# Optimization experiments

Measured on AMD Instinct MI355X. Metric: run time of the kernel, lower is better.

Reference implementation:

```python
import jax, jax.numpy as jnp
from jax import lax
import numpy as np

N_HOS, N_TYPES, N_STRUCTS = 4, 16, 512
N_COMBOS = N_HOS * N_TYPES  # 64
HID = 1024
N_ITERS = 60  # fixed PDHG iterations (differentiable unrolled solver)


def setup_inputs() -> dict:
    key = jax.random.key(0)
    ks = jax.random.split(key, 8)
    X = jax.random.uniform(ks[0], (2048, N_HOS, N_TYPES), dtype=jnp.float32)
    # sparse 0/1 structure matrix; guarantee each structure touches >=1 combo
    S = (jax.random.uniform(ks[1], (N_COMBOS, N_STRUCTS)) < 0.08).astype(jnp.float32)
    cols = jnp.arange(N_STRUCTS)
    S = S.at[cols % N_COMBOS, cols].set(1.0)
    # MLP params (He-ish init)
    W1 = jax.random.normal(ks[2], (N_COMBOS, HID), dtype=jnp.float32) * (2.0 / N_COMBOS) ** 0.5
    b1 = jnp.zeros((HID,), jnp.float32)
    W2 = jax.random.normal(ks[3], (HID, HID), dtype=jnp.float32) * (2.0 / HID) ** 0.5
    b2 = jnp.zeros((HID,), jnp.float32)
    W3 = jax.random.normal(ks[4], (HID, N_STRUCTS), dtype=jnp.float32) * (2.0 / HID) ** 0.5
    b3 = jnp.zeros((N_STRUCTS,), jnp.float32)
    return {"X": X, "W1": W1, "b1": b1, "W2": W2, "b2": b2,
            "W3": W3, "b3": b3, "S": S, "batch_size": 2048}


def nn_forward(X, W1, b1, W2, b2, W3, b3):
    # torch loop applies act_fun after EVERY layer, including the last
    Z = X.reshape(X.shape[0], -1)                 # [B, n_hos*n_types]
    Z = jax.nn.relu(Z @ W1 + b1)
    Z = jax.nn.relu(Z @ W2 + b2)
    Z = jax.nn.relu(Z @ W3 + b3)                  # [B, n_structures]
    return Z


def solve_lp(S, W, B, Z, n_iters=N_ITERS):
    """Batched solve of: max_x W.x - ||x - Z||_2  s.t. x >= 0, S x <= B.
    PDHG (Chambolle-Pock) on  min_x f(x) + i{Kx <= c},
    f(x) = -W.x + ||x - Z||_2,  K = [S; -I],  c = [B; 0].
    Same optimization problem as the CvxpyLayer, solved by a fixed-iteration
    batched primal-dual method (differentiable via unrolling)."""
    batch, n = Z.shape
    m = S.shape[0]

    # ||K||_2 via power iteration on K^T K = S^T S + I (constant wrt params)
    def pow_step(v, _):
        v2 = S.T @ (S @ v) + v
        return v2 / jnp.linalg.norm(v2), None
    v0 = jnp.full((n,), 1.0 / np.sqrt(n), Z.dtype)
    v, _ = lax.scan(pow_step, v0, None, length=30)
    L = jnp.sqrt(jnp.vdot(v, S.T @ (S @ v) + v))
    L = lax.stop_gradient(L)
    tau = 0.9 / L
    sigma = 0.9 / L

    c = jnp.concatenate([B, jnp.zeros_like(Z)], axis=-1)  # [B, m+n]

    def Kx(x):
        return jnp.concatenate([x @ S.T, -x], axis=-1)    # [B, m+n]

    def KTy(y):
        return y[:, :m] @ S - y[:, m:]                    # [B, n]

    def prox_f(v):
        # argmin_x 1/(2 tau) ||x - v||^2 - W.x + ||x - Z||_2
        u = v + tau * W
        d = u - Z
        nrm = jnp.linalg.norm(d, axis=-1, keepdims=True)
        scale = jnp.maximum(1.0 - tau / jnp.maximum(nrm, 1e-12), 0.0)
        return Z + scale * d

    def step(carry, _):
        x, xbar, y = carry
        y = jnp.maximum(y + sigma * (Kx(xbar) - c), 0.0)
        x_new = prox_f(x - tau * KTy(y))
        xbar = 2.0 * x_new - x
        return (x_new, xbar, y), None

    x0 = jnp.zeros_like(Z)
    y0 = jnp.zeros((batch, m + n), Z.dtype)
    (x, _, _), _ = lax.scan(step, (x0, x0, y0), None, length=n_iters)
    return x


def reference(X, W1, b1, W2, b2, W3, b3, S, batch_size):
    Z = nn_forward(X, W1, b1, W2, b2, W3, b3)     # [B, n_structures]
    W = jnp.ones_like(Z)                          # weights w = 1 (as in torch)
    B = X.reshape(batch_size, -1)                 # capacities b
    return solve_lp(S, W, B, Z)
```

## Files before the change

### kernel.cpp

```cpp
#include <hip/hip_runtime.h>


typedef _Float16 half8 __attribute__((ext_vector_type(8)));
typedef __fp16 fp16x2 __attribute__((ext_vector_type(2)));
typedef __fp16 fp16x4 __attribute__((ext_vector_type(4)));
typedef float floatx4 __attribute__((ext_vector_type(4)));
typedef float floatx2 __attribute__((ext_vector_type(2)));

#define BATCH 2048
#define NITERS 60
#define XBS 520
#define YLS 72

typedef const __attribute__((address_space(1))) unsigned int* gptr_as1;
typedef __attribute__((address_space(3))) unsigned int* lptr_as3;
__device__ __forceinline__ void gl_lds16(const _Float16* g, _Float16* s) {
    __builtin_amdgcn_global_load_lds((gptr_as1)g, (lptr_as3)s, 16, 0, 0);
}

template <int CTRL>
__device__ __forceinline__ float dpp_addf(float x) {
    int y = __builtin_amdgcn_update_dpp(0, __builtin_bit_cast(int, x), CTRL, 0xf, 0xf, true);
    return x + __builtin_bit_cast(float, y);
}
__device__ __forceinline__ float sum16(float x) {
    x = dpp_addf<0xB1>(x);
    x = dpp_addf<0x4E>(x);
    x = dpp_addf<0x124>(x);
    x = dpp_addf<0x128>(x);
    return x;
}
__device__ __forceinline__ float sum64(float x) {
    x = sum16(x);
    x += __builtin_bit_cast(float, __builtin_amdgcn_ds_swizzle(__builtin_bit_cast(int, x), 0x401F));
    x += __shfl_xor(x, 32, 64);
    return x;
}

__device__ void power_64(const float* __restrict__ S, float* __restrict__ tau_g) {
    __shared__ unsigned long long rowm[64][8];
    __shared__ float G[64][65];
    __shared__ float wl[64], pg[4][64];
    int t = threadIdx.x, wv = t >> 6, ln = t & 63;
    for (int rr = 0; rr < 16; rr++) {
        int r = wv * 16 + rr;
        float v[8];
#pragma unroll
        for (int e = 0; e < 8; e++) v[e] = S[r * 512 + e * 64 + ln];
#pragma unroll
        for (int e = 0; e < 8; e++) {
            unsigned long long m = __ballot(v[e] != 0.f);
            if (ln == 0) rowm[r][e] = m;
        }
    }
    __syncthreads();
    for (int k = 0; k < 16; k++) {
        int idx = t * 16 + k;
        int i = idx >> 6, j = idx & 63;
        int cnt = 0;
#pragma unroll
        for (int e = 0; e < 8; e++) cnt += __popcll(rowm[i][e] & rowm[j][e]);
        G[i][j] = (float)cnt;
    }
    if (wv == 0) {
        int cnt = 0;
#pragma unroll
        for (int e = 0; e < 8; e++) cnt += __popcll(rowm[ln][e]);
        wl[ln] = (float)cnt * 0.044194173824159216f;
    }
    __syncthreads();
    for (int s = 0; s < 30; s++) {
        float a = 0.f;
#pragma unroll
        for (int jj = 0; jj < 16; jj++) {
            int j = wv * 16 + jj;
            a += G[ln][j] * wl[j];
        }
        pg[wv][ln] = a;
        __syncthreads();
        if (wv == 0) {
            float g = (pg[0][ln] + pg[1][ln]) + (pg[2][ln] + pg[3][ln]);
            float wi = wl[ln];
            float s1 = sum64(wi * g);
            float s2 = sum64(wi * wi);
            float n = sqrtf(s1 + 2.f * s2 + 1.f);
            wl[ln] = (g + wi) / n;
        }
        __syncthreads();
    }
    if (wv == 0) {
        float wi = wl[ln];
        float s2 = sum64(wi * wi);
        if (ln == 0) tau_g[0] = 0.9f / sqrtf(s2 + 1.f);
    }
}

__global__ __launch_bounds__(256) void prep(
    const float* __restrict__ X, _Float16* __restrict__ Xh,
    const float* __restrict__ W1, _Float16* __restrict__ W1t,
    const float* __restrict__ W2, _Float16* __restrict__ W2t,
    const float* __restrict__ W3, _Float16* __restrict__ W3t,
    const float* __restrict__ S, _Float16* __restrict__ s1f,
    _Float16* __restrict__ s2f) {
    __shared__ float tile[32][33];
    int tid = threadIdx.x;
    int bid = blockIdx.x;
    if (bid < 512) {
        int i = bid * 256 + tid;
        Xh[i] = (_Float16)X[i];
        return;
    }
    bid -= 512;
    if (bid < 1600) {
        const float* W; _Float16* Wt; int K, N, b;
        if (bid < 64)        { W = W1; Wt = W1t; K = 64;   N = 1024; b = bid; }
        else if (bid < 1088) { W = W2; Wt = W2t; K = 1024; N = 1024; b = bid - 64; }
        else                 { W = W3; Wt = W3t; K = 1024; N = 512;  b = bid - 1088; }
        int nbx = N / 32;
        int n0 = (b % nbx) * 32, k0 = (b / nbx) * 32;
        int tx = tid & 31, ty = tid >> 5;
#pragma unroll
        for (int i = 0; i < 4; i++)
            tile[ty + i * 8][tx] = W[(size_t)(k0 + ty + i * 8) * N + n0 + tx];
        __syncthreads();
#pragma unroll
        for (int i = 0; i < 4; i++)
            Wt[(size_t)(n0 + ty + i * 8) * K + k0 + tx] = (_Float16)tile[tx][ty + i * 8];
        return;
    }
    bid -= 1600;
    int i = bid * 256 + tid;
    if (i < 4 * 16 * 64 * 8) {
        int j = i & 7, lane = (i >> 3) & 63, kk = (i >> 9) & 15, wc = i >> 13;
        int pos = kk * 32 + (lane >> 4) * 8 + j;
        int pp = pos >> 7, r = pos & 127;
        int hh = r >> 6, r2 = r & 63;
        int lmc = r2 >> 2, t3 = r2 & 3;
        int c = pp * 128 + (hh * 4 + t3) * 16 + lmc;
        int m = wc * 16 + (lane & 15);
        s1f[i] = (_Float16)S[m * 512 + c];
    } else {
        int i2 = i - 4 * 16 * 64 * 8;
        int j = i2 & 7, lane = (i2 >> 3) & 63, c = (i2 >> 9) & 1,
            tt = (i2 >> 10) & 7, wc = i2 >> 13;
        int kc = c * 32 + (lane >> 4) * 8 + j;
        int n = wc * 128 + tt * 16 + (lane & 15);
        s2f[i2] = (_Float16)S[kc * 512 + n];
    }
}

__global__ __launch_bounds__(256, 2) void gemm_relu(
    const _Float16* __restrict__ A, const _Float16* __restrict__ Wt,
    const float* __restrict__ bias, _Float16* __restrict__ outh,
    float* __restrict__ outf, int N, int K,
    const float* __restrict__ Sp, float* __restrict__ tau_g) {
    __shared__ __align__(16) _Float16 As[64 * 32];
    __shared__ __align__(16) _Float16 Bs[64 * 32];
    int tid = threadIdx.x;
    int bm = blockIdx.y * 64;
    int bn = blockIdx.x * 64;
    if (bn >= N) {
        if (blockIdx.y == 0 && Sp) power_64(Sp, tau_g);
        return;
    }
    int w = tid >> 6, l = tid & 63;
    int wr = w >> 1, wc = w & 1;
    int lm = l & 15, q = l >> 4;
    floatx4 acc[2][2] = {};

    int lc = l ^ ((l >> 3) & 7);
    int srow = w * 16 + (lc >> 2), scol = (lc & 3) * 8;
    const _Float16* ag = A + (size_t)(bm + srow) * K + scol;
    const _Float16* bg = Wt + (size_t)(bn + srow) * K + scol;
    _Float16* as = &As[(w * 16) * 32];
    _Float16* bs = &Bs[(w * 16) * 32];
    int sx = ((lm >> 1) & 7) << 3;

    for (int k0 = 0; k0 < K; k0 += 32) {
        gl_lds16(ag + k0, as);
        gl_lds16(bg + k0, bs);
        __syncthreads();
        half8 af[2], bf[2];
#pragma unroll
        for (int mt = 0; mt < 2; mt++)
            af[mt] = *(const half8*)&As[((wr * 32 + mt * 16 + lm) * 32 + q * 8) ^ sx];
#pragma unroll
        for (int nt = 0; nt < 2; nt++)
            bf[nt] = *(const half8*)&Bs[((wc * 32 + nt * 16 + lm) * 32 + q * 8) ^ sx];
#pragma unroll
        for (int mt = 0; mt < 2; mt++)
#pragma unroll
            for (int nt = 0; nt < 2; nt++)
                acc[mt][nt] = __builtin_amdgcn_mfma_f32_16x16x32_f16(
                    af[mt], bf[nt], acc[mt][nt], 0, 0, 0);
        __syncthreads();
    }
#pragma unroll
    for (int nt = 0; nt < 2; nt++) {
        int col = bn + wc * 32 + nt * 16 + lm;
        float bv = bias[col];
#pragma unroll
        for (int mt = 0; mt < 2; mt++) {
#pragma unroll
            for (int v = 0; v < 4; v++) {
                int row = bm + wr * 32 + mt * 16 + q * 4 + v;
                float val = fmaxf(acc[mt][nt][v] + bv, 0.f);
                if (outh) outh[(size_t)row * N + col] = (_Float16)val;
                else      outf[(size_t)row * N + col] = val;
            }
        }
    }
}

__global__ __launch_bounds__(256, 1) void pdhg_mfma(
    const float* __restrict__ Zb, const float* __restrict__ Xf,
    const _Float16* __restrict__ s1f, const _Float16* __restrict__ s2f,
    const float* __restrict__ tau_p, float* __restrict__ out) {
    __shared__ __align__(16) _Float16 xb_d[8 * XBS];
    __shared__ __align__(16) _Float16 yl_d[8 * YLS];
    __shared__ __align__(16) float red[8][4];
    int tid = threadIdx.x;
    int p = tid >> 6;
    int l = tid & 63, lm = l & 15, q = l >> 4;
    int lq = lm & 7;
    int qa = q & 1;
    int h = q >> 1;
    int b0 = blockIdx.x * 8;

    half8 s1[16], s2[8][2];
#pragma unroll
    for (int k = 0; k < 16; k++)
        s1[k] = *(const half8*)&s1f[((p * 16 + k) * 64 + l) * 8];
#pragma unroll
    for (int u = 0; u < 8; u++)
#pragma unroll
        for (int c = 0; c < 2; c++)
            s2[u][c] = *(const half8*)&s2f[(((p * 8 + u) * 2 + c) * 64 + l) * 8];

    floatx4 z4[4], tz4[4], x4[4], xb4[4], yh4[4], d4[4];
    floatx4 ylo = {}, Bc;
    floatx4 a1p[4] = {};
    floatx4 acc2[8] = {};
    const floatx4 zero4 = {0.f, 0.f, 0.f, 0.f};
    float tau = tau_p[0];
    float sig = tau;

#pragma unroll
    for (int v = 0; v < 4; v++)
        Bc[v] = Xf[(b0 + qa * 4 + v) * 64 + p * 16 + lm];
#pragma unroll
    for (int t = 0; t < 4; t++) {
#pragma unroll
        for (int v = 0; v < 4; v++) {
            float zz = Zb[(size_t)(b0 + qa * 4 + v) * 512 + p * 128 + (h * 4 + t) * 16 + lm];
            z4[t][v] = zz;
            tz4[t][v] = tau - zz;
        }
        x4[t] = zero4; xb4[t] = zero4; yh4[t] = zero4;
    }
    {
        half8 hz = {0, 0, 0, 0, 0, 0, 0, 0};
        for (int i = tid; i < (8 * XBS) / 8; i += 256)
            *(half8*)&xb_d[i * 8] = hz;
        for (int i = tid; i < 8 * YLS; i += 256)
            yl_d[i] = (_Float16)0.f;
    }
    __syncthreads();

#pragma unroll 1
    for (int it = 0; it < NITERS; ++it) {
#pragma unroll
        for (int k = 0; k < 16; k++) {
            half8 ad = *(const half8*)&xb_d[lq * XBS + k * 32 + q * 8];
            a1p[k & 3] = __builtin_amdgcn_mfma_f32_16x16x32_f16(ad, s1[k], a1p[k & 3], 0, 0, 0);
        }
        floatx4 a1 = (a1p[0] + a1p[1]) + (a1p[2] + a1p[3]);
        floatx4 yv = __builtin_elementwise_max(ylo + sig * (a1 - Bc), zero4);
        floatx4 dy = yv - ylo;
        ylo = yv;
        if (q < 2) {
#pragma unroll
            for (int v = 0; v < 4; v++)
                yl_d[(q * 4 + v) * YLS + p * 16 + lm] = (_Float16)dy[v];
        }
        __syncthreads();
        half8 a2d[2];
#pragma unroll
        for (int c = 0; c < 2; c++)
            a2d[c] = *(const half8*)&yl_d[lq * YLS + c * 32 + q * 8];
#pragma unroll
        for (int u = 0; u < 8; u++)
#pragma unroll
            for (int c = 0; c < 2; c++)
                acc2[u] = __builtin_amdgcn_mfma_f32_16x16x32_f16(a2d[c], s2[u][c], acc2[u], 0, 0, 0);
        floatx4 pn = {};
#pragma unroll
        for (int t = 0; t < 4; t++) {
            floatx4 accs = h ? acc2[t + 4] : acc2[t];
            yh4[t] = __builtin_elementwise_max(yh4[t] - sig * xb4[t], zero4);
            floatx4 kty = accs - yh4[t];
            floatx4 dd = (x4[t] - tau * kty) + tz4[t];
            d4[t] = dd;
            pn += dd * dd;
        }
#pragma unroll
        for (int v = 0; v < 4; v++) pn[v] = sum16(pn[v]);
#pragma unroll
        for (int v = 0; v < 4; v++) pn[v] += __shfl_xor(pn[v], 32, 64);
        if (lm == 0 && q < 2) {
#pragma unroll
            for (int v = 0; v < 4; v++) red[q * 4 + v][p] = pn[v];
        }
        __syncthreads();
        floatx4 sv;
#pragma unroll
        for (int v = 0; v < 4; v++) {
            floatx4 rr = *(const floatx4*)&red[qa * 4 + v][0];
            float n2 = (rr.x + rr.y) + (rr.z + rr.w);
            sv[v] = fmaxf(1.f - tau * rsqrtf(fmaxf(n2, 1e-24f)), 0.f);
        }
#pragma unroll
        for (int t = 0; t < 4; t++) {
            floatx4 xn = z4[t] + sv * d4[t];
            floatx4 xbn = 2.f * xn - x4[t];
            d4[t] = xbn - xb4[t];
            x4[t] = xn;
            xb4[t] = xbn;
        }
#pragma unroll
        for (int v = 0; v < 4; v++) {
            fp16x2 p0 = __builtin_amdgcn_cvt_pkrtz(d4[0][v], d4[1][v]);
            fp16x2 p1 = __builtin_amdgcn_cvt_pkrtz(d4[2][v], d4[3][v]);
            fp16x4 hd = __builtin_shufflevector(p0, p1, 0, 1, 2, 3);
            *(fp16x4*)&xb_d[(qa * 4 + v) * XBS + p * 128 + h * 64 + lm * 4] = hd;
        }
        __syncthreads();
    }
#pragma unroll
    for (int t = 0; t < 4; t++)
#pragma unroll
        for (int v = 0; v < 4; v++)
            out[(size_t)(b0 + qa * 4 + v) * 512 + p * 128 + (h * 4 + t) * 16 + lm] = x4[t][v];
}

extern "C" void kernel_launch(void* const* d_in, const int* in_sizes, int n_in,
                              void* d_out, int out_size, void* d_ws, size_t ws_size,
                              hipStream_t stream) {
    const float* X  = (const float*)d_in[0];
    const float* W1 = (const float*)d_in[1];
    const float* b1 = (const float*)d_in[2];
    const float* W2 = (const float*)d_in[3];
    const float* b2 = (const float*)d_in[4];
    const float* W3 = (const float*)d_in[5];
    const float* b3 = (const float*)d_in[6];
    const float* S  = (const float*)d_in[7];
    float* out = (float*)d_out;

    char* ws = (char*)d_ws;
    size_t off = 0;
    auto alloc = [&](size_t bytes) {
        void* p = ws + off;
        off += (bytes + 255) & ~(size_t)255;
        return p;
    };
    _Float16* Xh  = (_Float16*)alloc((size_t)BATCH * 64 * 2);
    _Float16* W1t = (_Float16*)alloc((size_t)64 * 1024 * 2);
    _Float16* W2t = (_Float16*)alloc((size_t)1024 * 1024 * 2);
    _Float16* W3t = (_Float16*)alloc((size_t)1024 * 512 * 2);
    _Float16* H1  = (_Float16*)alloc((size_t)BATCH * 1024 * 2);
    _Float16* H2  = (_Float16*)alloc((size_t)BATCH * 1024 * 2);
    float*    Zb  = (float*)alloc((size_t)BATCH * 512 * 4);
    _Float16* s1f = (_Float16*)alloc((size_t)4 * 16 * 64 * 8 * 2);
    _Float16* s2f = (_Float16*)alloc((size_t)4 * 8 * 2 * 64 * 8 * 2);
    float*    tau = (float*)alloc(256);

    hipLaunchKernelGGL(prep, dim3(2368), dim3(256), 0, stream,
                       X, Xh, W1, W1t, W2, W2t, W3, W3t, S, s1f, s2f);
    hipLaunchKernelGGL(gemm_relu, dim3(16, 32), dim3(256), 0, stream,
                       Xh, W1t, b1, H1, (float*)nullptr, 1024, 64,
                       (const float*)nullptr, (float*)nullptr);
    hipLaunchKernelGGL(gemm_relu, dim3(17, 32), dim3(256), 0, stream,
                       H1, W2t, b2, H2, (float*)nullptr, 1024, 1024, S, tau);
    hipLaunchKernelGGL(gemm_relu, dim3(8, 32), dim3(256), 0, stream,
                       H2, W3t, b3, (_Float16*)nullptr, Zb, 512, 1024,
                       (const float*)nullptr, (float*)nullptr);
    hipLaunchKernelGGL(pdhg_mfma, dim3(BATCH / 8), dim3(256), 0, stream,
                       Zb, X, s1f, s2f, tau, out);
}
```

Measured before the change: 204.2 us.

## Fuse first MLP layer and power iteration into prep kernel, double-buffer GEMM

Computes the first MLP layer directly from fp32 X and W1 inside the prep kernel, converting to fp16 on the fly into LDS. This removes the separate X and W1 conversion passes and one kernel launch. The power iteration that computes tau moves into the same prep kernel instead of occupying an extra column of blocks in the layer-2 GEMM. The remaining GEMMs gain double-buffered LDS so the next K slab loads while MFMAs run on the current one. The cost is one fewer barrier-free overlap point and more LDS per block, which may lower occupancy.

```diff
diff --git a/kernel.cpp b/kernel.cpp
--- a/kernel.cpp
+++ b/kernel.cpp
@@ -37,10 +37,13 @@
     return x;
 }
 
-__device__ void power_64(const float* __restrict__ S, float* __restrict__ tau_g) {
-    __shared__ unsigned long long rowm[64][8];
-    __shared__ float G[64][65];
-    __shared__ float wl[64], pg[4][64];
+__device__ void power_64(const float* __restrict__ S, float* __restrict__ tau_g,
+                         char* smem) {
+    typedef unsigned long long ull;
+    ull (*rowm)[8] = (ull(*)[8])smem;
+    float (*G)[65] = (float(*)[65])(smem + 4096);
+    float* wl = (float*)(smem + 4096 + 16640);
+    float (*pg)[64] = (float(*)[64])(smem + 4096 + 16640 + 256);
     int t = threadIdx.x, wv = t >> 6, ln = t & 63;
     for (int rr = 0; rr < 16; rr++) {
         int r = wv * 16 + rr;
@@ -95,27 +98,81 @@
     }
 }
 
-__global__ __launch_bounds__(256) void prep(
-    const float* __restrict__ X, _Float16* __restrict__ Xh,
-    const float* __restrict__ W1, _Float16* __restrict__ W1t,
+__global__ __launch_bounds__(256) void head(
+    const float* __restrict__ X, const float* __restrict__ W1,
+    const float* __restrict__ b1, _Float16* __restrict__ H1,
     const float* __restrict__ W2, _Float16* __restrict__ W2t,
     const float* __restrict__ W3, _Float16* __restrict__ W3t,
     const float* __restrict__ S, _Float16* __restrict__ s1f,
-    _Float16* __restrict__ s2f) {
-    __shared__ float tile[32][33];
+    _Float16* __restrict__ s2f, float* __restrict__ tau_g) {
+    __shared__ __align__(16) char smem[22272];
     int tid = threadIdx.x;
     int bid = blockIdx.x;
     if (bid < 512) {
-        int i = bid * 256 + tid;
-        Xh[i] = (_Float16)X[i];
+        _Float16* As = (_Float16*)smem;
+        _Float16* Bs = (_Float16*)(smem + 8192);
+        int bm = (bid >> 4) * 64, bn = (bid & 15) * 64;
+        {
+            int r = tid >> 2, c0 = (tid & 3) * 16;
+            const float* xp = X + (size_t)(bm + r) * 64 + c0;
+            int sw = (r & 7) << 3;
+#pragma unroll
+            for (int i = 0; i < 4; i++) {
+                floatx4 v = *(const floatx4*)(xp + i * 4);
+                fp16x4 hh = {(__fp16)v.x, (__fp16)v.y, (__fp16)v.z, (__fp16)v.w};
+                *(fp16x4*)&As[r * 64 + ((c0 + i * 4) ^ sw)] = hh;
+            }
+            int nx = tid & 63, ky = (tid >> 6) * 16;
+            int swb = (nx & 7) << 3;
+#pragma unroll
+            for (int i = 0; i < 16; i++) {
+                float wv = W1[(size_t)(ky + i) * 1024 + bn + nx];
+                Bs[nx * 64 + ((ky + i) ^ swb)] = (_Float16)wv;
+            }
+        }
+        __syncthreads();
+        int w = tid >> 6, l = tid & 63;
+        int wr = w >> 1, wc = w & 1;
+        int lm = l & 15, q = l >> 4;
+        int sxa = (lm & 7) << 3;
+        floatx4 acc[2][2] = {};
+#pragma unroll
+        for (int k0 = 0; k0 < 64; k0 += 32) {
+            half8 af[2], bf[2];
+#pragma unroll
+            for (int mt = 0; mt < 2; mt++)
+                af[mt] = *(const half8*)&As[(wr * 32 + mt * 16 + lm) * 64 + ((k0 + q * 8) ^ sxa)];
+#pragma unroll
+            for (int nt = 0; nt < 2; nt++)
+                bf[nt] = *(const half8*)&Bs[(wc * 32 + nt * 16 + lm) * 64 + ((k0 + q * 8) ^ sxa)];
+#pragma unroll
+            for (int mt = 0; mt < 2; mt++)
+#pragma unroll
+                for (int nt = 0; nt < 2; nt++)
+                    acc[mt][nt] = __builtin_amdgcn_mfma_f32_16x16x32_f16(
+                        af[mt], bf[nt], acc[mt][nt], 0, 0, 0);
+        }
+#pragma unroll
+        for (int nt = 0; nt < 2; nt++) {
+            int col = bn + wc * 32 + nt * 16 + lm;
+            float bv = b1[col];
+#pragma unroll
+            for (int mt = 0; mt < 2; mt++)
+#pragma unroll
+                for (int v = 0; v < 4; v++) {
+                    int row = bm + wr * 32 + mt * 16 + q * 4 + v;
+                    H1[(size_t)row * 1024 + col] =
+                        (_Float16)fmaxf(acc[mt][nt][v] + bv, 0.f);
+                }
+        }
         return;
     }
     bid -= 512;
-    if (bid < 1600) {
+    if (bid < 1536) {
+        float (*tile)[33] = (float(*)[33])smem;
         const float* W; _Float16* Wt; int K, N, b;
-        if (bid < 64)        { W = W1; Wt = W1t; K = 64;   N = 1024; b = bid; }
-        else if (bid < 1088) { W = W2; Wt = W2t; K = 1024; N = 1024; b = bid - 64; }
-        else                 { W = W3; Wt = W3t; K = 1024; N = 512;  b = bid - 1088; }
+        if (bid < 1024) { W = W2; Wt = W2t; K = 1024; N = 1024; b = bid; }
+        else            { W = W3; Wt = W3t; K = 1024; N = 512;  b = bid - 1024; }
         int nbx = N / 32;
         int n0 = (b % nbx) * 32, k0 = (b / nbx) * 32;
         int tx = tid & 31, ty = tid >> 5;
@@ -128,41 +185,40 @@
             Wt[(size_t)(n0 + ty + i * 8) * K + k0 + tx] = (_Float16)tile[tx][ty + i * 8];
         return;
     }
-    bid -= 1600;
-    int i = bid * 256 + tid;
-    if (i < 4 * 16 * 64 * 8) {
-        int j = i & 7, lane = (i >> 3) & 63, kk = (i >> 9) & 15, wc = i >> 13;
-        int pos = kk * 32 + (lane >> 4) * 8 + j;
-        int pp = pos >> 7, r = pos & 127;
-        int hh = r >> 6, r2 = r & 63;
-        int lmc = r2 >> 2, t3 = r2 & 3;
-        int c = pp * 128 + (hh * 4 + t3) * 16 + lmc;
-        int m = wc * 16 + (lane & 15);
-        s1f[i] = (_Float16)S[m * 512 + c];
-    } else {
-        int i2 = i - 4 * 16 * 64 * 8;
-        int j = i2 & 7, lane = (i2 >> 3) & 63, c = (i2 >> 9) & 1,
-            tt = (i2 >> 10) & 7, wc = i2 >> 13;
-        int kc = c * 32 + (lane >> 4) * 8 + j;
-        int n = wc * 128 + tt * 16 + (lane & 15);
-        s2f[i2] = (_Float16)S[kc * 512 + n];
-    }
-}
-
-__global__ __launch_bounds__(256, 2) void gemm_relu(
+    bid -= 1536;
+    if (bid < 256) {
+        int i = bid * 256 + tid;
+        if (i < 4 * 16 * 64 * 8) {
+            int j = i & 7, lane = (i >> 3) & 63, kk = (i >> 9) & 15, wc = i >> 13;
+            int pos = kk * 32 + (lane >> 4) * 8 + j;
+            int pp = pos >> 7, r = pos & 127;
+            int hh = r >> 6, r2 = r & 63;
+            int lmc = r2 >> 2, t3 = r2 & 3;
+            int c = pp * 128 + (hh * 4 + t3) * 16 + lmc;
+            int m = wc * 16 + (lane & 15);
+            s1f[i] = (_Float16)S[m * 512 + c];
+        } else {
+            int i2 = i - 4 * 16 * 64 * 8;
+            int j = i2 & 7, lane = (i2 >> 3) & 63, c = (i2 >> 9) & 1,
+                tt = (i2 >> 10) & 7, wc = i2 >> 13;
+            int kc = c * 32 + (lane >> 4) * 8 + j;
+            int n = wc * 128 + tt * 16 + (lane & 15);
+            s2f[i2] = (_Float16)S[kc * 512 + n];
+        }
+        return;
+    }
+    power_64(S, tau_g, smem);
+}
+
+__global__ __launch_bounds__(256, 2) void gemm_relu_db(
     const _Float16* __restrict__ A, const _Float16* __restrict__ Wt,
     const float* __restrict__ bias, _Float16* __restrict__ outh,
-    float* __restrict__ outf, int N, int K,
-    const float* __restrict__ Sp, float* __restrict__ tau_g) {
-    __shared__ __align__(16) _Float16 As[64 * 32];
-    __shared__ __align__(16) _Float16 Bs[64 * 32];
+    float* __restrict__ outf, int N, int K) {
+    __shared__ __align__(16) _Float16 As[2][64 * 32];
+    __shared__ __align__(16) _Float16 Bs[2][64 * 32];
     int tid = threadIdx.x;
     int bm = blockIdx.y * 64;
     int bn = blockIdx.x * 64;
-    if (bn >= N) {
-        if (blockIdx.y == 0 && Sp) power_64(Sp, tau_g);
-        return;
-    }
     int w = tid >> 6, l = tid & 63;
     int wr = w >> 1, wc = w & 1;
     int lm = l & 15, q = l >> 4;
@@ -172,27 +228,53 @@
     int srow = w * 16 + (lc >> 2), scol = (lc & 3) * 8;
     const _Float16* ag = A + (size_t)(bm + srow) * K + scol;
     const _Float16* bg = Wt + (size_t)(bn + srow) * K + scol;
-    _Float16* as = &As[(w * 16) * 32];
-    _Float16* bs = &Bs[(w * 16) * 32];
+    _Float16* as0 = &As[0][(w * 16) * 32];
+    _Float16* bs0 = &Bs[0][(w * 16) * 32];
+    _Float16* as1 = &As[1][(w * 16) * 32];
+    _Float16* bs1 = &Bs[1][(w * 16) * 32];
     int sx = ((lm >> 1) & 7) << 3;
 
-    for (int k0 = 0; k0 < K; k0 += 32) {
-        gl_lds16(ag + k0, as);
-        gl_lds16(bg + k0, bs);
-        __syncthreads();
-        half8 af[2], bf[2];
-#pragma unroll
-        for (int mt = 0; mt < 2; mt++)
-            af[mt] = *(const half8*)&As[((wr * 32 + mt * 16 + lm) * 32 + q * 8) ^ sx];
-#pragma unroll
-        for (int nt = 0; nt < 2; nt++)
-            bf[nt] = *(const half8*)&Bs[((wc * 32 + nt * 16 + lm) * 32 + q * 8) ^ sx];
-#pragma unroll
-        for (int mt = 0; mt < 2; mt++)
+    gl_lds16(ag, as0);
+    gl_lds16(bg, bs0);
+    __syncthreads();
+    for (int k0 = 0; k0 < K; k0 += 64) {
+        gl_lds16(ag + k0 + 32, as1);
+        gl_lds16(bg + k0 + 32, bs1);
+        {
+            half8 af[2], bf[2];
+#pragma unroll
+            for (int mt = 0; mt < 2; mt++)
+                af[mt] = *(const half8*)&As[0][((wr * 32 + mt * 16 + lm) * 32 + q * 8) ^ sx];
 #pragma unroll
             for (int nt = 0; nt < 2; nt++)
-                acc[mt][nt] = __builtin_amdgcn_mfma_f32_16x16x32_f16(
-                    af[mt], bf[nt], acc[mt][nt], 0, 0, 0);
+                bf[nt] = *(const half8*)&Bs[0][((wc * 32 + nt * 16 + lm) * 32 + q * 8) ^ sx];
+#pragma unroll
+            for (int mt = 0; mt < 2; mt++)
+#pragma unroll
+                for (int nt = 0; nt < 2; nt++)
+                    acc[mt][nt] = __builtin_amdgcn_mfma_f32_16x16x32_f16(
+                        af[mt], bf[nt], acc[mt][nt], 0, 0, 0);
+        }
+        __syncthreads();
+        if (k0 + 64 < K) {
+            gl_lds16(ag + k0 + 64, as0);
+            gl_lds16(bg + k0 + 64, bs0);
+        }
+        {
+            half8 af[2], bf[2];
+#pragma unroll
+            for (int mt = 0; mt < 2; mt++)
+                af[mt] = *(const half8*)&As[1][((wr * 32 + mt * 16 + lm) * 32 + q * 8) ^ sx];
+#pragma unroll
+            for (int nt = 0; nt < 2; nt++)
+                bf[nt] = *(const half8*)&Bs[1][((wc * 32 + nt * 16 + lm) * 32 + q * 8) ^ sx];
+#pragma unroll
+            for (int mt = 0; mt < 2; mt++)
+#pragma unroll
+                for (int nt = 0; nt < 2; nt++)
+                    acc[mt][nt] = __builtin_amdgcn_mfma_f32_16x16x32_f16(
+                        af[mt], bf[nt], acc[mt][nt], 0, 0, 0);
+        }
         __syncthreads();
     }
 #pragma unroll
@@ -363,8 +445,6 @@
         off += (bytes + 255) & ~(size_t)255;
         return p;
     };
-    _Float16* Xh  = (_Float16*)alloc((size_t)BATCH * 64 * 2);
-    _Float16* W1t = (_Float16*)alloc((size_t)64 * 1024 * 2);
     _Float16* W2t = (_Float16*)alloc((size_t)1024 * 1024 * 2);
     _Float16* W3t = (_Float16*)alloc((size_t)1024 * 512 * 2);
     _Float16* H1  = (_Float16*)alloc((size_t)BATCH * 1024 * 2);
@@ -374,16 +454,12 @@
     _Float16* s2f = (_Float16*)alloc((size_t)4 * 8 * 2 * 64 * 8 * 2);
     float*    tau = (float*)alloc(256);
 
-    hipLaunchKernelGGL(prep, dim3(2368), dim3(256), 0, stream,
-                       X, Xh, W1, W1t, W2, W2t, W3, W3t, S, s1f, s2f);
-    hipLaunchKernelGGL(gemm_relu, dim3(16, 32), dim3(256), 0, stream,
-                       Xh, W1t, b1, H1, (float*)nullptr, 1024, 64,
-                       (const float*)nullptr, (float*)nullptr);
-    hipLaunchKernelGGL(gemm_relu, dim3(17, 32), dim3(256), 0, stream,
-                       H1, W2t, b2, H2, (float*)nullptr, 1024, 1024, S, tau);
-    hipLaunchKernelGGL(gemm_relu, dim3(8, 32), dim3(256), 0, stream,
-                       H2, W3t, b3, (_Float16*)nullptr, Zb, 512, 1024,
-                       (const float*)nullptr, (float*)nullptr);
+    hipLaunchKernelGGL(head, dim3(2305), dim3(256), 0, stream,
+                       X, W1, b1, H1, W2, W2t, W3, W3t, S, s1f, s2f, tau);
+    hipLaunchKernelGGL(gemm_relu_db, dim3(16, 32), dim3(256), 0, stream,
+                       H1, W2t, b2, H2, (float*)nullptr, 1024, 1024);
+    hipLaunchKernelGGL(gemm_relu_db, dim3(8, 32), dim3(256), 0, stream,
+                       H2, W3t, b3, (_Float16*)nullptr, Zb, 512, 1024);
     hipLaunchKernelGGL(pdhg_mfma, dim3(BATCH / 8), dim3(256), 0, stream,
                        Zb, X, s1f, s2f, tau, out);
 }
```

Result: slower. 213.3 us (+4.5%).

## Fuse MLP layers into the PDHG kernel per 8-row batch tile

Applied to the files above, without the earlier changes.

Removes the three separate GEMM launches and the fp16 X conversion. Each 8-row PDHG block now computes its own MLP forward pass: H1 and H2 live in shared memory, and the final layer's output stays in registers as Z. This removes global round-trips for H1, H2 and Z and cuts kernel launches. The cost is that every block streams the full W2t and W3t matrices straight from global memory without LDS staging, and half of each 16-row MFMA tile is unused. The power iteration moves into the prep kernel as an extra block.

```diff
diff --git a/kernel.cpp b/kernel.cpp
--- a/kernel.cpp
+++ b/kernel.cpp
@@ -5,18 +5,12 @@
 typedef __fp16 fp16x2 __attribute__((ext_vector_type(2)));
 typedef __fp16 fp16x4 __attribute__((ext_vector_type(4)));
 typedef float floatx4 __attribute__((ext_vector_type(4)));
-typedef float floatx2 __attribute__((ext_vector_type(2)));
 
 #define BATCH 2048
 #define NITERS 60
 #define XBS 520
 #define YLS 72
-
-typedef const __attribute__((address_space(1))) unsigned int* gptr_as1;
-typedef __attribute__((address_space(3))) unsigned int* lptr_as3;
-__device__ __forceinline__ void gl_lds16(const _Float16* g, _Float16* s) {
-    __builtin_amdgcn_global_load_lds((gptr_as1)g, (lptr_as3)s, 16, 0, 0);
-}
+#define H1S 1032
 
 template <int CTRL>
 __device__ __forceinline__ float dpp_addf(float x) {
@@ -96,21 +90,14 @@
 }
 
 __global__ __launch_bounds__(256) void prep(
-    const float* __restrict__ X, _Float16* __restrict__ Xh,
     const float* __restrict__ W1, _Float16* __restrict__ W1t,
     const float* __restrict__ W2, _Float16* __restrict__ W2t,
     const float* __restrict__ W3, _Float16* __restrict__ W3t,
     const float* __restrict__ S, _Float16* __restrict__ s1f,
-    _Float16* __restrict__ s2f) {
+    _Float16* __restrict__ s2f, float* __restrict__ tau_g) {
     __shared__ float tile[32][33];
     int tid = threadIdx.x;
     int bid = blockIdx.x;
-    if (bid < 512) {
-        int i = bid * 256 + tid;
-        Xh[i] = (_Float16)X[i];
-        return;
-    }
-    bid -= 512;
     if (bid < 1600) {
         const float* W; _Float16* Wt; int K, N, b;
         if (bid < 64)        { W = W1; Wt = W1t; K = 64;   N = 1024; b = bid; }
@@ -128,114 +115,149 @@
             Wt[(size_t)(n0 + ty + i * 8) * K + k0 + tx] = (_Float16)tile[tx][ty + i * 8];
         return;
     }
-    bid -= 1600;
-    int i = bid * 256 + tid;
-    if (i < 4 * 16 * 64 * 8) {
-        int j = i & 7, lane = (i >> 3) & 63, kk = (i >> 9) & 15, wc = i >> 13;
-        int pos = kk * 32 + (lane >> 4) * 8 + j;
-        int pp = pos >> 7, r = pos & 127;
-        int hh = r >> 6, r2 = r & 63;
-        int lmc = r2 >> 2, t3 = r2 & 3;
-        int c = pp * 128 + (hh * 4 + t3) * 16 + lmc;
-        int m = wc * 16 + (lane & 15);
-        s1f[i] = (_Float16)S[m * 512 + c];
-    } else {
-        int i2 = i - 4 * 16 * 64 * 8;
-        int j = i2 & 7, lane = (i2 >> 3) & 63, c = (i2 >> 9) & 1,
-            tt = (i2 >> 10) & 7, wc = i2 >> 13;
-        int kc = c * 32 + (lane >> 4) * 8 + j;
-        int n = wc * 128 + tt * 16 + (lane & 15);
-        s2f[i2] = (_Float16)S[kc * 512 + n];
-    }
-}
-
-__global__ __launch_bounds__(256, 2) void gemm_relu(
-    const _Float16* __restrict__ A, const _Float16* __restrict__ Wt,
-    const float* __restrict__ bias, _Float16* __restrict__ outh,
-    float* __restrict__ outf, int N, int K,
-    const float* __restrict__ Sp, float* __restrict__ tau_g) {
-    __shared__ __align__(16) _Float16 As[64 * 32];
-    __shared__ __align__(16) _Float16 Bs[64 * 32];
-    int tid = threadIdx.x;
-    int bm = blockIdx.y * 64;
-    int bn = blockIdx.x * 64;
-    if (bn >= N) {
-        if (blockIdx.y == 0 && Sp) power_64(Sp, tau_g);
+    if (bid < 1856) {
+        int i = (bid - 1600) * 256 + tid;
+        if (i < 4 * 16 * 64 * 8) {
+            int j = i & 7, lane = (i >> 3) & 63, kk = (i >> 9) & 15, wc = i >> 13;
+            int pos = kk * 32 + (lane >> 4) * 8 + j;
+            int pp = pos >> 7, r = pos & 127;
+            int hh = r >> 6, r2 = r & 63;
+            int lmc = r2 >> 2, t3 = r2 & 3;
+            int c = pp * 128 + (hh * 4 + t3) * 16 + lmc;
+            int m = wc * 16 + (lane & 15);
+            s1f[i] = (_Float16)S[m * 512 + c];
+        } else {
+            int i2 = i - 4 * 16 * 64 * 8;
+            int j = i2 & 7, lane = (i2 >> 3) & 63, c = (i2 >> 9) & 1,
+                tt = (i2 >> 10) & 7, wc = i2 >> 13;
+            int kc = c * 32 + (lane >> 4) * 8 + j;
+            int n = wc * 128 + tt * 16 + (lane & 15);
+            s2f[i2] = (_Float16)S[kc * 512 + n];
+        }
         return;
     }
-    int w = tid >> 6, l = tid & 63;
-    int wr = w >> 1, wc = w & 1;
-    int lm = l & 15, q = l >> 4;
-    floatx4 acc[2][2] = {};
-
-    int lc = l ^ ((l >> 3) & 7);
-    int srow = w * 16 + (lc >> 2), scol = (lc & 3) * 8;
-    const _Float16* ag = A + (size_t)(bm + srow) * K + scol;
-    const _Float16* bg = Wt + (size_t)(bn + srow) * K + scol;
-    _Float16* as = &As[(w * 16) * 32];
-    _Float16* bs = &Bs[(w * 16) * 32];
-    int sx = ((lm >> 1) & 7) << 3;
-
-    for (int k0 = 0; k0 < K; k0 += 32) {
-        gl_lds16(ag + k0, as);
-        gl_lds16(bg + k0, bs);
-        __syncthreads();
-        half8 af[2], bf[2];
-#pragma unroll
-        for (int mt = 0; mt < 2; mt++)
-            af[mt] = *(const half8*)&As[((wr * 32 + mt * 16 + lm) * 32 + q * 8) ^ sx];
-#pragma unroll
-        for (int nt = 0; nt < 2; nt++)
-            bf[nt] = *(const half8*)&Bs[((wc * 32 + nt * 16 + lm) * 32 + q * 8) ^ sx];
-#pragma unroll
-        for (int mt = 0; mt < 2; mt++)
-#pragma unroll
-            for (int nt = 0; nt < 2; nt++)
-                acc[mt][nt] = __builtin_amdgcn_mfma_f32_16x16x32_f16(
-                    af[mt], bf[nt], acc[mt][nt], 0, 0, 0);
-        __syncthreads();
-    }
-#pragma unroll
-    for (int nt = 0; nt < 2; nt++) {
-        int col = bn + wc * 32 + nt * 16 + lm;
-        float bv = bias[col];
-#pragma unroll
-        for (int mt = 0; mt < 2; mt++) {
-#pragma unroll
-            for (int v = 0; v < 4; v++) {
-                int row = bm + wr * 32 + mt * 16 + q * 4 + v;
-                float val = fmaxf(acc[mt][nt][v] + bv, 0.f);
-                if (outh) outh[(size_t)row * N + col] = (_Float16)val;
-                else      outf[(size_t)row * N + col] = val;
-            }
-        }
-    }
-}
-
-__global__ __launch_bounds__(256, 1) void pdhg_mfma(
-    const float* __restrict__ Zb, const float* __restrict__ Xf,
+    power_64(S, tau_g);
+}
+
+__global__ __launch_bounds__(256, 1) void mega(
+    const float* __restrict__ X,
+    const _Float16* __restrict__ W1t, const float* __restrict__ b1,
+    const _Float16* __restrict__ W2t, const float* __restrict__ b2,
+    const _Float16* __restrict__ W3t, const float* __restrict__ b3,
     const _Float16* __restrict__ s1f, const _Float16* __restrict__ s2f,
     const float* __restrict__ tau_p, float* __restrict__ out) {
-    __shared__ __align__(16) _Float16 xb_d[8 * XBS];
-    __shared__ __align__(16) _Float16 yl_d[8 * YLS];
-    __shared__ __align__(16) float red[8][4];
+    __shared__ __align__(16) char smem[34304];
+    _Float16* H1 = (_Float16*)smem;
+    _Float16* H2 = (_Float16*)(smem + 16512);
+    _Float16* X8 = (_Float16*)(smem + 33024);
+    _Float16* xb_d = (_Float16*)smem;
+    _Float16* yl_d = (_Float16*)(smem + 8320);
+    float (*red)[4] = (float(*)[4])(smem + 9472);
+
     int tid = threadIdx.x;
-    int p = tid >> 6;
+    int wp = tid >> 6;
     int l = tid & 63, lm = l & 15, q = l >> 4;
     int lq = lm & 7;
-    int qa = q & 1;
-    int h = q >> 1;
+    int qa = q & 1, h = q >> 1;
     int b0 = blockIdx.x * 8;
 
+    if (tid < 128) {
+        int r = tid >> 4, c = (tid & 15) * 4;
+        floatx4 v = *(const floatx4*)&X[(size_t)(b0 + r) * 64 + c];
+        fp16x4 hh = {(__fp16)v.x, (__fp16)v.y, (__fp16)v.z, (__fp16)v.w};
+        *(fp16x4*)&X8[r * 72 + c] = hh;
+    }
+    __syncthreads();
+
+    {
+        floatx4 acc1[16] = {};
+#pragma unroll
+        for (int kk = 0; kk < 2; kk++) {
+            half8 a = *(const half8*)&X8[lq * 72 + kk * 32 + q * 8];
+#pragma unroll
+            for (int u = 0; u < 16; u++) {
+                int col = wp * 256 + u * 16 + lm;
+                half8 b = *(const half8*)&W1t[(size_t)col * 64 + kk * 32 + q * 8];
+                acc1[u] = __builtin_amdgcn_mfma_f32_16x16x32_f16(a, b, acc1[u], 0, 0, 0);
+            }
+        }
+        if (q < 2) {
+#pragma unroll
+            for (int u = 0; u < 16; u++) {
+                int col = wp * 256 + u * 16 + lm;
+                float bv = b1[col];
+#pragma unroll
+                for (int v = 0; v < 4; v++)
+                    H1[(q * 4 + v) * H1S + col] = (_Float16)fmaxf(acc1[u][v] + bv, 0.f);
+            }
+        }
+    }
+    __syncthreads();
+
+    {
+        floatx4 acc2h[16] = {};
+        half8 B2[16];
+#pragma unroll
+        for (int u = 0; u < 16; u++)
+            B2[u] = *(const half8*)&W2t[(size_t)(wp * 256 + u * 16 + lm) * 1024 + q * 8];
+        half8 a_cur = *(const half8*)&H1[lq * H1S + q * 8];
+#pragma unroll 1
+        for (int k0 = 0; k0 < 1024; k0 += 32) {
+            int knx = (k0 + 32) & 1023;
+            half8 a_nxt = *(const half8*)&H1[lq * H1S + knx + q * 8];
+#pragma unroll
+            for (int u = 0; u < 16; u++) {
+                half8 bn = *(const half8*)&W2t[(size_t)(wp * 256 + u * 16 + lm) * 1024 + knx + q * 8];
+                acc2h[u] = __builtin_amdgcn_mfma_f32_16x16x32_f16(a_cur, B2[u], acc2h[u], 0, 0, 0);
+                B2[u] = bn;
+            }
+            a_cur = a_nxt;
+        }
+        __syncthreads();
+        if (q < 2) {
+#pragma unroll
+            for (int u = 0; u < 16; u++) {
+                int col = wp * 256 + u * 16 + lm;
+                float bv = b2[col];
+#pragma unroll
+                for (int v = 0; v < 4; v++)
+                    H2[(q * 4 + v) * H1S + col] = (_Float16)fmaxf(acc2h[u][v] + bv, 0.f);
+            }
+        }
+    }
+    __syncthreads();
+
+    floatx4 acc3[8] = {};
+    {
+        half8 B3[8];
+#pragma unroll
+        for (int u = 0; u < 8; u++)
+            B3[u] = *(const half8*)&W3t[(size_t)(wp * 128 + u * 16 + lm) * 1024 + q * 8];
+        half8 a_cur = *(const half8*)&H2[lq * H1S + q * 8];
+#pragma unroll 1
+        for (int k0 = 0; k0 < 1024; k0 += 32) {
+            int knx = (k0 + 32) & 1023;
+            half8 a_nxt = *(const half8*)&H2[lq * H1S + knx + q * 8];
+#pragma unroll
+            for (int u = 0; u < 8; u++) {
+                half8 bn = *(const half8*)&W3t[(size_t)(wp * 128 + u * 16 + lm) * 1024 + knx + q * 8];
+                acc3[u] = __builtin_amdgcn_mfma_f32_16x16x32_f16(a_cur, B3[u], acc3[u], 0, 0, 0);
+                B3[u] = bn;
+            }
+            a_cur = a_nxt;
+        }
+    }
+    __syncthreads();
+
     half8 s1[16], s2[8][2];
 #pragma unroll
     for (int k = 0; k < 16; k++)
-        s1[k] = *(const half8*)&s1f[((p * 16 + k) * 64 + l) * 8];
+        s1[k] = *(const half8*)&s1f[((wp * 16 + k) * 64 + l) * 8];
 #pragma unroll
     for (int u = 0; u < 8; u++)
 #pragma unroll
         for (int c = 0; c < 2; c++)
-            s2[u][c] = *(const half8*)&s2f[(((p * 8 + u) * 2 + c) * 64 + l) * 8];
+            s2[u][c] = *(const half8*)&s2f[(((wp * 8 + u) * 2 + c) * 64 + l) * 8];
 
     floatx4 z4[4], tz4[4], x4[4], xb4[4], yh4[4], d4[4];
     floatx4 ylo = {}, Bc;
@@ -247,12 +269,14 @@
 
 #pragma unroll
     for (int v = 0; v < 4; v++)
-        Bc[v] = Xf[(b0 + qa * 4 + v) * 64 + p * 16 + lm];
+        Bc[v] = X[(size_t)(b0 + qa * 4 + v) * 64 + wp * 16 + lm];
 #pragma unroll
     for (int t = 0; t < 4; t++) {
+        int col = wp * 128 + (h * 4 + t) * 16 + lm;
+        float bv = b3[col];
 #pragma unroll
         for (int v = 0; v < 4; v++) {
-            float zz = Zb[(size_t)(b0 + qa * 4 + v) * 512 + p * 128 + (h * 4 + t) * 16 + lm];
+            float zz = fmaxf(acc3[h * 4 + t][v] + bv, 0.f);
             z4[t][v] = zz;
             tz4[t][v] = tau - zz;
         }
@@ -281,7 +305,7 @@
         if (q < 2) {
 #pragma unroll
             for (int v = 0; v < 4; v++)
-                yl_d[(q * 4 + v) * YLS + p * 16 + lm] = (_Float16)dy[v];
+                yl_d[(q * 4 + v) * YLS + wp * 16 + lm] = (_Float16)dy[v];
         }
         __syncthreads();
         half8 a2d[2];
@@ -309,7 +333,7 @@
         for (int v = 0; v < 4; v++) pn[v] += __shfl_xor(pn[v], 32, 64);
         if (lm == 0 && q < 2) {
 #pragma unroll
-            for (int v = 0; v < 4; v++) red[q * 4 + v][p] = pn[v];
+            for (int v = 0; v < 4; v++) red[q * 4 + v][wp] = pn[v];
         }
         __syncthreads();
         floatx4 sv;
@@ -332,7 +356,7 @@
             fp16x2 p0 = __builtin_amdgcn_cvt_pkrtz(d4[0][v], d4[1][v]);
             fp16x2 p1 = __builtin_amdgcn_cvt_pkrtz(d4[2][v], d4[3][v]);
             fp16x4 hd = __builtin_shufflevector(p0, p1, 0, 1, 2, 3);
-            *(fp16x4*)&xb_d[(qa * 4 + v) * XBS + p * 128 + h * 64 + lm * 4] = hd;
+            *(fp16x4*)&xb_d[(qa * 4 + v) * XBS + wp * 128 + h * 64 + lm * 4] = hd;
         }
         __syncthreads();
     }
@@ -340,7 +364,7 @@
     for (int t = 0; t < 4; t++)
 #pragma unroll
         for (int v = 0; v < 4; v++)
-            out[(size_t)(b0 + qa * 4 + v) * 512 + p * 128 + (h * 4 + t) * 16 + lm] = x4[t][v];
+            out[(size_t)(b0 + qa * 4 + v) * 512 + wp * 128 + (h * 4 + t) * 16 + lm] = x4[t][v];
 }
 
 extern "C" void kernel_launch(void* const* d_in, const int* in_sizes, int n_in,
@@ -363,27 +387,15 @@
         off += (bytes + 255) & ~(size_t)255;
         return p;
     };
-    _Float16* Xh  = (_Float16*)alloc((size_t)BATCH * 64 * 2);
     _Float16* W1t = (_Float16*)alloc((size_t)64 * 1024 * 2);
     _Float16* W2t = (_Float16*)alloc((size_t)1024 * 1024 * 2);
     _Float16* W3t = (_Float16*)alloc((size_t)1024 * 512 * 2);
-    _Float16* H1  = (_Float16*)alloc((size_t)BATCH * 1024 * 2);
-    _Float16* H2  = (_Float16*)alloc((size_t)BATCH * 1024 * 2);
-    float*    Zb  = (float*)alloc((size_t)BATCH * 512 * 4);
     _Float16* s1f = (_Float16*)alloc((size_t)4 * 16 * 64 * 8 * 2);
     _Float16* s2f = (_Float16*)alloc((size_t)4 * 8 * 2 * 64 * 8 * 2);
     float*    tau = (float*)alloc(256);
 
-    hipLaunchKernelGGL(prep, dim3(2368), dim3(256), 0, stream,
-                       X, Xh, W1, W1t, W2, W2t, W3, W3t, S, s1f, s2f);
-    hipLaunchKernelGGL(gemm_relu, dim3(16, 32), dim3(256), 0, stream,
-                       Xh, W1t, b1, H1, (float*)nullptr, 1024, 64,
-                       (const float*)nullptr, (float*)nullptr);
-    hipLaunchKernelGGL(gemm_relu, dim3(17, 32), dim3(256), 0, stream,
-                       H1, W2t, b2, H2, (float*)nullptr, 1024, 1024, S, tau);
-    hipLaunchKernelGGL(gemm_relu, dim3(8, 32), dim3(256), 0, stream,
-                       H2, W3t, b3, (_Float16*)nullptr, Zb, 512, 1024,
-                       (const float*)nullptr, (float*)nullptr);
-    hipLaunchKernelGGL(pdhg_mfma, dim3(BATCH / 8), dim3(256), 0, stream,
-                       Zb, X, s1f, s2f, tau, out);
-}
+    hipLaunchKernelGGL(prep, dim3(1857), dim3(256), 0, stream,
+                       W1, W1t, W2, W2t, W3, W3t, S, s1f, s2f, tau);
+    hipLaunchKernelGGL(mega, dim3(BATCH / 8), dim3(256), 0, stream,
+                       X, W1t, b1, W2t, b2, W3t, b3, s1f, s2f, tau, out);
+}
```

Result: slower. 279.7 us (+37.0%).

## Fuse prep and three MLP GEMMs into one cooperative persistent kernel

Applied to the files above, without the earlier changes.

Replaces the prep kernel and three gemm_relu launches with a single cooperative kernel of 512 blocks that does conversion and transposes, grid-syncs, then runs each GEMM layer in turn with grid syncs between layers. The aim is to remove launch overhead and inter-kernel gaps. In exchange the grid is fixed at 512 blocks, so the third GEMM uses only half the blocks, and power iteration now runs serially on one block before the first grid sync instead of overlapping with GEMM2. That serial power iteration could lengthen the critical path.

```diff
diff --git a/kernel.cpp b/kernel.cpp
--- a/kernel.cpp
+++ b/kernel.cpp
@@ -1,11 +1,13 @@
 #include <hip/hip_runtime.h>
+#include <hip/hip_cooperative_groups.h>
+
+namespace cg = cooperative_groups;
 
 
 typedef _Float16 half8 __attribute__((ext_vector_type(8)));
 typedef __fp16 fp16x2 __attribute__((ext_vector_type(2)));
 typedef __fp16 fp16x4 __attribute__((ext_vector_type(4)));
 typedef float floatx4 __attribute__((ext_vector_type(4)));
-typedef float floatx2 __attribute__((ext_vector_type(2)));
 
 #define BATCH 2048
 #define NITERS 60
@@ -37,10 +39,13 @@
     return x;
 }
 
-__device__ void power_64(const float* __restrict__ S, float* __restrict__ tau_g) {
-    __shared__ unsigned long long rowm[64][8];
-    __shared__ float G[64][65];
-    __shared__ float wl[64], pg[4][64];
+__device__ void power_64s(const float* __restrict__ S, float* __restrict__ tau_g,
+                          char* smem) {
+    typedef unsigned long long ull;
+    ull (*rowm)[8] = (ull(*)[8])smem;
+    float (*G)[65] = (float(*)[65])(smem + 4096);
+    float* wl = (float*)(smem + 4096 + 16640);
+    float (*pg)[64] = (float(*)[64])(smem + 4096 + 16640 + 256);
     int t = threadIdx.x, wv = t >> 6, ln = t & 63;
     for (int rr = 0; rr < 16; rr++) {
         int r = wv * 16 + rr;
@@ -95,74 +100,29 @@
     }
 }
 
-__global__ __launch_bounds__(256) void prep(
-    const float* __restrict__ X, _Float16* __restrict__ Xh,
-    const float* __restrict__ W1, _Float16* __restrict__ W1t,
-    const float* __restrict__ W2, _Float16* __restrict__ W2t,
-    const float* __restrict__ W3, _Float16* __restrict__ W3t,
-    const float* __restrict__ S, _Float16* __restrict__ s1f,
-    _Float16* __restrict__ s2f) {
-    __shared__ float tile[32][33];
-    int tid = threadIdx.x;
-    int bid = blockIdx.x;
-    if (bid < 512) {
-        int i = bid * 256 + tid;
-        Xh[i] = (_Float16)X[i];
-        return;
-    }
-    bid -= 512;
-    if (bid < 1600) {
-        const float* W; _Float16* Wt; int K, N, b;
-        if (bid < 64)        { W = W1; Wt = W1t; K = 64;   N = 1024; b = bid; }
-        else if (bid < 1088) { W = W2; Wt = W2t; K = 1024; N = 1024; b = bid - 64; }
-        else                 { W = W3; Wt = W3t; K = 1024; N = 512;  b = bid - 1088; }
-        int nbx = N / 32;
-        int n0 = (b % nbx) * 32, k0 = (b / nbx) * 32;
-        int tx = tid & 31, ty = tid >> 5;
-#pragma unroll
-        for (int i = 0; i < 4; i++)
-            tile[ty + i * 8][tx] = W[(size_t)(k0 + ty + i * 8) * N + n0 + tx];
-        __syncthreads();
-#pragma unroll
-        for (int i = 0; i < 4; i++)
-            Wt[(size_t)(n0 + ty + i * 8) * K + k0 + tx] = (_Float16)tile[tx][ty + i * 8];
-        return;
-    }
-    bid -= 1600;
-    int i = bid * 256 + tid;
-    if (i < 4 * 16 * 64 * 8) {
-        int j = i & 7, lane = (i >> 3) & 63, kk = (i >> 9) & 15, wc = i >> 13;
-        int pos = kk * 32 + (lane >> 4) * 8 + j;
-        int pp = pos >> 7, r = pos & 127;
-        int hh = r >> 6, r2 = r & 63;
-        int lmc = r2 >> 2, t3 = r2 & 3;
-        int c = pp * 128 + (hh * 4 + t3) * 16 + lmc;
-        int m = wc * 16 + (lane & 15);
-        s1f[i] = (_Float16)S[m * 512 + c];
-    } else {
-        int i2 = i - 4 * 16 * 64 * 8;
-        int j = i2 & 7, lane = (i2 >> 3) & 63, c = (i2 >> 9) & 1,
-            tt = (i2 >> 10) & 7, wc = i2 >> 13;
-        int kc = c * 32 + (lane >> 4) * 8 + j;
-        int n = wc * 128 + tt * 16 + (lane & 15);
-        s2f[i2] = (_Float16)S[kc * 512 + n];
-    }
-}
-
-__global__ __launch_bounds__(256, 2) void gemm_relu(
+__device__ __forceinline__ void transpose32(const float* __restrict__ W,
+                                            _Float16* __restrict__ Wt,
+                                            int K, int N, int b, char* smem) {
+    float (*tile)[33] = (float(*)[33])smem;
+    int nbx = N / 32;
+    int n0 = (b % nbx) * 32, k0 = (b / nbx) * 32;
+    int tx = threadIdx.x & 31, ty = threadIdx.x >> 5;
+#pragma unroll
+    for (int i = 0; i < 4; i++)
+        tile[ty + i * 8][tx] = W[(size_t)(k0 + ty + i * 8) * N + n0 + tx];
+    __syncthreads();
+#pragma unroll
+    for (int i = 0; i < 4; i++)
+        Wt[(size_t)(n0 + ty + i * 8) * K + k0 + tx] = (_Float16)tile[tx][ty + i * 8];
+}
+
+__device__ void gemm_tile(
     const _Float16* __restrict__ A, const _Float16* __restrict__ Wt,
     const float* __restrict__ bias, _Float16* __restrict__ outh,
-    float* __restrict__ outf, int N, int K,
-    const float* __restrict__ Sp, float* __restrict__ tau_g) {
-    __shared__ __align__(16) _Float16 As[64 * 32];
-    __shared__ __align__(16) _Float16 Bs[64 * 32];
+    float* __restrict__ outf, int N, int K, int bm, int bn, char* smem) {
+    _Float16* As = (_Float16*)smem;
+    _Float16* Bs = (_Float16*)(smem + 4096);
     int tid = threadIdx.x;
-    int bm = blockIdx.y * 64;
-    int bn = blockIdx.x * 64;
-    if (bn >= N) {
-        if (blockIdx.y == 0 && Sp) power_64(Sp, tau_g);
-        return;
-    }
     int w = tid >> 6, l = tid & 63;
     int wr = w >> 1, wc = w & 1;
     int lm = l & 15, q = l >> 4;
@@ -210,6 +170,79 @@
             }
         }
     }
+}
+
+__global__ __launch_bounds__(256, 2) void fused(
+    const float* __restrict__ X, _Float16* __restrict__ Xh,
+    const float* __restrict__ W1, _Float16* __restrict__ W1t,
+    const float* __restrict__ W2, _Float16* __restrict__ W2t,
+    const float* __restrict__ W3, _Float16* __restrict__ W3t,
+    const float* __restrict__ S, _Float16* __restrict__ s1f,
+    _Float16* __restrict__ s2f, const float* __restrict__ b1,
+    _Float16* __restrict__ H1, const float* __restrict__ b2,
+    _Float16* __restrict__ H2, const float* __restrict__ b3,
+    float* __restrict__ Zb, float* __restrict__ tau_g) {
+    __shared__ __align__(16) char smem[22016];
+    cg::grid_group grid = cg::this_grid();
+    int tid = threadIdx.x;
+    int bid = blockIdx.x;
+
+    {
+        int i = bid * 256 + tid;
+        Xh[i] = (_Float16)X[i];
+    }
+    auto do_t = [&](int j) {
+        const float* W; _Float16* Wt; int K, N, b;
+        if (j < 64)        { W = W1; Wt = W1t; K = 64;   N = 1024; b = j; }
+        else if (j < 1088) { W = W2; Wt = W2t; K = 1024; N = 1024; b = j - 64; }
+        else               { W = W3; Wt = W3t; K = 1024; N = 512;  b = j - 1088; }
+        transpose32(W, Wt, K, N, b, smem);
+    };
+    do_t(bid);
+    __syncthreads();
+    do_t(bid + 512);
+    __syncthreads();
+    do_t(bid + 1024);
+    if (bid < 64) {
+        __syncthreads();
+        do_t(bid + 1536);
+    }
+    if (bid < 256) {
+        int i = bid * 256 + tid;
+        if (i < 4 * 16 * 64 * 8) {
+            int j = i & 7, lane = (i >> 3) & 63, kk = (i >> 9) & 15, wc = i >> 13;
+            int pos = kk * 32 + (lane >> 4) * 8 + j;
+            int pp = pos >> 7, r = pos & 127;
+            int hh = r >> 6, r2 = r & 63;
+            int lmc = r2 >> 2, t3 = r2 & 3;
+            int c = pp * 128 + (hh * 4 + t3) * 16 + lmc;
+            int m = wc * 16 + (lane & 15);
+            s1f[i] = (_Float16)S[m * 512 + c];
+        } else {
+            int i2 = i - 4 * 16 * 64 * 8;
+            int j = i2 & 7, lane = (i2 >> 3) & 63, c = (i2 >> 9) & 1,
+                tt = (i2 >> 10) & 7, wc = i2 >> 13;
+            int kc = c * 32 + (lane >> 4) * 8 + j;
+            int n = wc * 128 + tt * 16 + (lane & 15);
+            s2f[i2] = (_Float16)S[kc * 512 + n];
+        }
+    } else if (bid == 511) {
+        __syncthreads();
+        power_64s(S, tau_g, smem);
+    }
+    grid.sync();
+
+    gemm_tile(Xh, W1t, b1, H1, (float*)nullptr, 1024, 64,
+              (bid >> 4) * 64, (bid & 15) * 64, smem);
+    grid.sync();
+
+    gemm_tile(H1, W2t, b2, H2, (float*)nullptr, 1024, 1024,
+              (bid >> 4) * 64, (bid & 15) * 64, smem);
+    grid.sync();
+
+    if (bid < 256)
+        gemm_tile(H2, W3t, b3, (_Float16*)nullptr, Zb, 512, 1024,
+                  (bid >> 3) * 64, (bid & 7) * 64, smem);
 }
 
 __global__ __launch_bounds__(256, 1) void pdhg_mfma(
@@ -374,16 +407,13 @@
     _Float16* s2f = (_Float16*)alloc((size_t)4 * 8 * 2 * 64 * 8 * 2);
     float*    tau = (float*)alloc(256);
 
-    hipLaunchKernelGGL(prep, dim3(2368), dim3(256), 0, stream,
-                       X, Xh, W1, W1t, W2, W2t, W3, W3t, S, s1f, s2f);
-    hipLaunchKernelGGL(gemm_relu, dim3(16, 32), dim3(256), 0, stream,
-                       Xh, W1t, b1, H1, (float*)nullptr, 1024, 64,
-                       (const float*)nullptr, (float*)nullptr);
-    hipLaunchKernelGGL(gemm_relu, dim3(17, 32), dim3(256), 0, stream,
-                       H1, W2t, b2, H2, (float*)nullptr, 1024, 1024, S, tau);
-    hipLaunchKernelGGL(gemm_relu, dim3(8, 32), dim3(256), 0, stream,
-                       H2, W3t, b3, (_Float16*)nullptr, Zb, 512, 1024,
-                       (const float*)nullptr, (float*)nullptr);
+    void* args[] = {(void*)&X,  (void*)&Xh,  (void*)&W1, (void*)&W1t,
+                    (void*)&W2, (void*)&W2t, (void*)&W3, (void*)&W3t,
+                    (void*)&S,  (void*)&s1f, (void*)&s2f, (void*)&b1,
+                    (void*)&H1, (void*)&b2,  (void*)&H2, (void*)&b3,
+                    (void*)&Zb, (void*)&tau};
+    hipLaunchCooperativeKernel((void*)fused, dim3(512), dim3(256),
+                               args, 0, stream);
     hipLaunchKernelGGL(pdhg_mfma, dim3(BATCH / 8), dim3(256), 0, stream,
                        Zb, X, s1f, s2f, tau, out);
 }
```

After: 409.3 us. 100% more time.
